# Performance work log

Hardware: AMD Instinct MI355X
Metric: run time of the kernel (lower is better)

Reference implementation:

```python
import jax, jax.numpy as jnp
import numpy as np

D_MODEL = 2048
N_HEADS = 16
D_HEAD = 128
N_GROUPS = 4          # KV heads = N_HEADS // N_GROUPS = 4
D_FF = 2048           # hard-coded default in FeedForward
EPS = 1e-6


def setup_inputs() -> dict:
    key = jax.random.key(0)
    ks = jax.random.split(key, 16)
    B, S = 4, 1024
    Hkv = N_HEADS // N_GROUPS
    s = 0.02
    inp = {
        "x": jax.random.normal(ks[0], (B, S, D_MODEL), jnp.float32),
        "scale1": jnp.ones((D_MODEL,), jnp.float32),
        "Wq": jax.random.normal(ks[1], (D_MODEL, N_HEADS * D_HEAD), jnp.float32) * s,
        "bq": jnp.zeros((N_HEADS * D_HEAD,), jnp.float32),
        "Wk": jax.random.normal(ks[2], (D_MODEL, Hkv * D_HEAD), jnp.float32) * s,
        "bk": jnp.zeros((Hkv * D_HEAD,), jnp.float32),
        "Wv": jax.random.normal(ks[3], (D_MODEL, Hkv * D_HEAD), jnp.float32) * s,
        "bv": jnp.zeros((Hkv * D_HEAD,), jnp.float32),
        "Wo": jax.random.normal(ks[4], (N_HEADS * D_HEAD, D_MODEL), jnp.float32) * s,
        "bo": jnp.zeros((D_MODEL,), jnp.float32),
        "W1": jax.random.normal(ks[5], (D_MODEL, D_FF), jnp.float32) * s,
        "b1": jnp.zeros((D_FF,), jnp.float32),
        "W2": jax.random.normal(ks[6], (D_FF, D_MODEL), jnp.float32) * s,
        "b2": jnp.zeros((D_MODEL,), jnp.float32),
    }
    return inp


def _rmsnorm(x, scale):
    rms = jnp.sqrt(jnp.mean(x * x, axis=-1, keepdims=True) + EPS)
    return scale * (x / rms)


def reference(x, scale1, Wq, bq, Wk, bk, Wv, bv, Wo, bo, W1, b1, W2, b2):
    B, S, _ = x.shape
    Hkv = N_HEADS // N_GROUPS
    xn = _rmsnorm(x, scale1)  # [B,S,D]

    # GQA attention (prefill, step=None -> no cache)
    Q = (xn @ Wq + bq).reshape(B, S, N_HEADS, D_HEAD).transpose(0, 2, 1, 3)  # [B,H,S,d]
    K = (xn @ Wk + bk).reshape(B, S, Hkv, D_HEAD).transpose(0, 2, 1, 3)      # [B,Hkv,S,d]
    V = (xn @ Wv + bv).reshape(B, S, Hkv, D_HEAD).transpose(0, 2, 1, 3)
    Kr = jnp.repeat(K, N_GROUPS, axis=1)  # [B,H,S,d]
    Vr = jnp.repeat(V, N_GROUPS, axis=1)
    scores = jnp.einsum("bhqd,bhkd->bhqk", Q, Kr) / jnp.sqrt(jnp.float32(D_HEAD))
    attn = jax.nn.softmax(scores, axis=-1)
    out = jnp.einsum("bhqk,bhkd->bhqd", attn, Vr)  # [B,H,S,d]
    out = out.transpose(0, 2, 1, 3).reshape(B, S, N_HEADS * D_HEAD)
    x = x + out @ Wo + bo

    # Source bug preserved: FFN consumes rms_norm1 output, rms_norm2 is dead code
    h = xn @ W1 + b1
    h = h * jax.nn.sigmoid(h) * h  # x_ff * silu(x_ff)
    x = x + h @ W2 + b2
    return x
```

## Files before the change

### kernel.cpp

```cpp
#include <hip/hip_runtime.h>
#include <hip/hip_bf16.h>
#include <cstdint>

using bf16 = __hip_bfloat16;
typedef __attribute__((ext_vector_type(8))) __bf16 bf16x8;
typedef __attribute__((ext_vector_type(4))) float f32x4;

#define MFMA16(a, b, c) __builtin_amdgcn_mfma_f32_16x16x32_bf16((a), (b), (c), 0, 0, 0)

#if __has_builtin(__builtin_amdgcn_exp2f)
__device__ __forceinline__ float fexp2(float x) { return __builtin_amdgcn_exp2f(x); }
#else
__device__ __forceinline__ float fexp2(float x) { return exp2f(x); }
#endif

__device__ __forceinline__ void async16(void* lds_ptr, const void* gptr) {
  auto g = reinterpret_cast<__attribute__((address_space(1))) unsigned int*>(
      reinterpret_cast<uintptr_t>(gptr));
  auto l = reinterpret_cast<__attribute__((address_space(3))) unsigned int*>(
      static_cast<unsigned int>(reinterpret_cast<uintptr_t>(lds_ptr)));
  __builtin_amdgcn_global_load_lds(g, l, 16, 0, 0);
}

__device__ __forceinline__ void tr_body(const float* __restrict__ W,
                                        bf16* __restrict__ Wt, int N, int ldt,
                                        int row_off, int k_off, int lb, int nx,
                                        float (*t)[33], int tx, int ty) {
  const int n0 = (lb % nx) * 32, k0 = (lb / nx) * 32;
#pragma unroll
  for (int i = 0; i < 4; ++i)
    t[ty + 8 * i][tx] = W[(size_t)(k0 + ty + 8 * i) * N + n0 + tx];
  __syncthreads();
#pragma unroll
  for (int i = 0; i < 4; ++i)
    Wt[(size_t)(row_off + n0 + ty + 8 * i) * ldt + k_off + k0 + tx] =
        __float2bfloat16(t[tx][ty + 8 * i]);
}

__global__ __launch_bounds__(256) void prep_k(
    const float* __restrict__ x, const float* __restrict__ s1, bf16* __restrict__ xn,
    const float* __restrict__ Wq, const float* __restrict__ Wk,
    const float* __restrict__ Wv, const float* __restrict__ W1,
    const float* __restrict__ Wo, const float* __restrict__ W2,
    bf16* __restrict__ wcatT, bf16* __restrict__ wcat2T,
    const float* __restrict__ bq, const float* __restrict__ bk,
    const float* __restrict__ bv, const float* __restrict__ b1,
    const float* __restrict__ bo, const float* __restrict__ b2,
    float* __restrict__ bcat) {
  __shared__ float t[32][33];
  const int tid = threadIdx.x;
  int bid = blockIdx.x;
  if (bid < 4096) {
    const int row = bid;
    const float4* xr = (const float4*)(x + (size_t)row * 2048);
    float4 a = xr[tid * 2], b = xr[tid * 2 + 1];
    float ss = a.x * a.x + a.y * a.y + a.z * a.z + a.w * a.w +
               b.x * b.x + b.y * b.y + b.z * b.z + b.w * b.w;
#pragma unroll
    for (int d = 1; d < 64; d <<= 1) ss += __shfl_xor(ss, d);
    if ((tid & 63) == 0) t[0][tid >> 6] = ss;
    __syncthreads();
    const float rinv =
        rsqrtf((t[0][0] + t[0][1] + t[0][2] + t[0][3]) * (1.0f / 2048.0f) + 1e-6f);
    const float4* sp = (const float4*)s1;
    float4 s0 = sp[tid * 2], s1v = sp[tid * 2 + 1];
    union { bf16 h[8]; bf16x8 v; } o;
    o.h[0] = __float2bfloat16(a.x * rinv * s0.x);
    o.h[1] = __float2bfloat16(a.y * rinv * s0.y);
    o.h[2] = __float2bfloat16(a.z * rinv * s0.z);
    o.h[3] = __float2bfloat16(a.w * rinv * s0.w);
    o.h[4] = __float2bfloat16(b.x * rinv * s1v.x);
    o.h[5] = __float2bfloat16(b.y * rinv * s1v.y);
    o.h[6] = __float2bfloat16(b.z * rinv * s1v.z);
    o.h[7] = __float2bfloat16(b.w * rinv * s1v.w);
    *(bf16x8*)(xn + (size_t)row * 2048 + tid * 8) = o.v;
    return;
  }
  if (bid < 4124) {
    const int i = (bid - 4096) * 256 + tid;
    float v;
    if (i < 2048) v = bq[i];
    else if (i < 2560) v = bk[i - 2048];
    else if (i < 3072) v = bv[i - 2560];
    else if (i < 5120) v = b1[i - 3072];
    else v = bo[i - 5120] + b2[i - 5120];
    bcat[i] = v;
    return;
  }
  bid -= 4124;
  const int tx = tid & 31, ty = tid >> 5;
  if (bid < 4096)       tr_body(Wq, wcatT, 2048, 2048, 0, 0, bid, 64, t, tx, ty);
  else if (bid < 5120)  tr_body(Wk, wcatT, 512, 2048, 2048, 0, bid - 4096, 16, t, tx, ty);
  else if (bid < 6144)  tr_body(Wv, wcatT, 512, 2048, 2560, 0, bid - 5120, 16, t, tx, ty);
  else if (bid < 10240) tr_body(W1, wcatT, 2048, 2048, 3072, 0, bid - 6144, 64, t, tx, ty);
  else if (bid < 14336) tr_body(Wo, wcat2T, 2048, 4096, 0, 0, bid - 10240, 64, t, tx, ty);
  else                  tr_body(W2, wcat2T, 2048, 4096, 0, 2048, bid - 14336, 64, t, tx, ty);
}

__global__ void transpose_v_k(const bf16* __restrict__ qkv, bf16* __restrict__ vtb) {
  __shared__ bf16 t[32][33];
  const int bh = blockIdx.z, b = bh >> 2, g = bh & 3;
  const int s0 = blockIdx.x * 32, d0 = blockIdx.y * 32;
  const int tx = threadIdx.x, ty = threadIdx.y;
#pragma unroll
  for (int i = 0; i < 4; ++i)
    t[ty + 8 * i][tx] =
        qkv[(size_t)(b * 1024 + s0 + ty + 8 * i) * 3072 + 2560 + g * 128 + d0 + tx];
  __syncthreads();
#pragma unroll
  for (int i = 0; i < 4; ++i)
    vtb[((size_t)bh * 128 + d0 + ty + 8 * i) * 1024 + s0 + tx] = t[tx][ty + 8 * i];
}

#define BARRIER() \
  { asm volatile("" ::: "memory"); __builtin_amdgcn_s_barrier(); asm volatile("" ::: "memory"); }
#define LGKM0() \
  { asm volatile("s_waitcnt lgkmcnt(0)" ::: "memory"); __builtin_amdgcn_sched_barrier(0); }
#define VM_MAIN                                                          \
  { if constexpr (LPS == 4) { asm volatile("s_waitcnt vmcnt(8)" ::: "memory"); } \
    else { asm volatile("s_waitcnt vmcnt(6)" ::: "memory"); }            \
    __builtin_amdgcn_sched_barrier(0); }
#define VM_ONE                                                           \
  { if constexpr (LPS == 4) { asm volatile("s_waitcnt vmcnt(4)" ::: "memory"); } \
    else { asm volatile("s_waitcnt vmcnt(3)" ::: "memory"); }            \
    __builtin_amdgcn_sched_barrier(0); }
#define VM_ZERO \
  { asm volatile("s_waitcnt vmcnt(0)" ::: "memory"); __builtin_amdgcn_sched_barrier(0); }

#define READ_AF(MILO)                                                              \
  { unsigned char* ab_ = lds + (h_ & 3) * SLOTA;                                   \
    _Pragma("unroll") for (int i_ = 0; i_ < MI / 2; ++i_) {                        \
      const int R_ = arow0 + ((MILO) + i_) * 16;                                   \
      af[i_] = *(const bf16x8*)(ab_ + R_ * 64 + ((hi ^ ((R_ >> 1) & 3)) << 4)); } }

#define READ_BF()                                                                  \
  { unsigned char* bb_ = lds + 4 * SLOTA + (h_ & 3) * SLOTB;                       \
    _Pragma("unroll") for (int j_ = 0; j_ < NJ; ++j_) {                            \
      const int S_ = bcol0 + j_ * 16;                                              \
      bf[j_] = *(const bf16x8*)(bb_ + S_ * 64 + ((hi ^ ((S_ >> 1) & 3)) << 4)); } }

#define MFMA_HALF(MILO)                                                            \
  __builtin_amdgcn_s_setprio(1);                                                   \
  _Pragma("unroll") for (int i_ = 0; i_ < MI / 2; ++i_)                            \
    _Pragma("unroll") for (int j_ = 0; j_ < NJ; ++j_)                              \
      acc[(MILO) + i_][j_] = MFMA16(af[i_], bf[j_], acc[(MILO) + i_][j_]);         \
  __builtin_amdgcn_s_setprio(0);

#define GSLOT(H, DOSTG, VMSTMT)                                                    \
  { const int h_ = (H);                                                            \
    READ_AF(0); READ_BF();                                                         \
    if (DOSTG) stgA(h_ + 3);                                                       \
    BARRIER(); LGKM0();                                                            \
    MFMA_HALF(0);                                                                  \
    BARRIER();                                                                     \
    READ_AF(MI / 2);                                                               \
    if (DOSTG) stgB(h_ + 3);                                                       \
    VMSTMT;                                                                        \
    BARRIER(); LGKM0();                                                            \
    MFMA_HALF(MI / 2);                                                             \
    BARRIER(); }

template <int MI, int NJ, int WM, int WN, int EPI>
__global__ __launch_bounds__(512, 2) void gemm8(
    const bf16* __restrict__ A, const bf16* __restrict__ A2,
    const bf16* __restrict__ Bt, const float* __restrict__ bias,
    const float* __restrict__ res, void* __restrict__ out0,
    void* __restrict__ out1, int K) {
  constexpr int BM = WM * MI * 16;
  constexpr int BN = WN * NJ * 16;
  constexpr int SLOTA = BM * 64;
  constexpr int SLOTB = BN * 64;
  constexpr int NSWA = SLOTA / 8192;
  constexpr int NSWB = SLOTB / 8192;
  constexpr int FRACB = SLOTB % 8192;
  constexpr int LPS = NSWA + NSWB;
  extern __shared__ unsigned char lds[];

  const int tid = threadIdx.x, lane = tid & 63, w = tid >> 6;
  const int wr = w / WN, wc = w % WN;
  const int hi = lane >> 4, lo = lane & 15;

  const int lid = blockIdx.y * 16 + blockIdx.x;
  const int xj = lid & 7, jj = lid >> 3;
  const int brow = ((xj & 3) * 4 + (jj & 3)) * BM;
  const int bcol = ((xj >> 2) * 8 + (jj >> 2)) * BN;

  const int NS = K >> 5;

  size_t offA[NSWA];
#pragma unroll
  for (int i = 0; i < NSWA; ++i) {
    const int o = i * 8192 + tid * 16;
    const int r = o >> 6;
    const int c = ((((o >> 4) & 3) ^ ((r >> 1) & 3)) << 3);
    offA[i] = (size_t)(brow + r) * 2048 + c;
  }
  const bf16* srcB[NSWB + (FRACB ? 1 : 0)];
#pragma unroll
  for (int i = 0; i < NSWB + (FRACB ? 1 : 0); ++i) {
    const int o = i * 8192 + tid * 16;
    const int r = o >> 6;
    const int c = ((((o >> 4) & 3) ^ ((r >> 1) & 3)) << 3);
    srcB[i] = Bt + (size_t)(bcol + r) * K + c;
  }

  auto stgA = [&](int h) {
    unsigned char* ab = lds + (h & 3) * SLOTA;
    const int kb = h * 32;
    const bf16* base;
    int ko;
    if constexpr (EPI == 1) { base = (kb < 2048) ? A : A2; ko = kb & 2047; }
    else { base = A; ko = kb; }
#pragma unroll
    for (int i = 0; i < NSWA; ++i)
      async16(ab + i * 8192 + tid * 16, base + offA[i] + ko);
  };
  auto stgB = [&](int h) {
    unsigned char* bb = lds + 4 * SLOTA + (h & 3) * SLOTB;
    const int kb = h * 32;
#pragma unroll
    for (int i = 0; i < NSWB; ++i)
      async16(bb + i * 8192 + tid * 16, srcB[i] + kb);
    if constexpr (FRACB != 0) {
      if (tid < FRACB / 16)
        async16(bb + NSWB * 8192 + tid * 16, srcB[NSWB] + kb);
    }
  };

  const int arow0 = wr * (MI * 16) + lo;
  const int bcol0 = wc * (NJ * 16) + lo;

  stgA(0); stgB(0); stgA(1); stgB(1); stgA(2); stgB(2);
  VM_MAIN;
  BARRIER();

  f32x4 acc[MI][NJ] = {};
  bf16x8 af[MI / 2], bf[NJ];

  for (int h = 0; h < NS - 3; ++h) { GSLOT(h, true, VM_MAIN); }
  GSLOT(NS - 3, false, VM_ONE);
  GSLOT(NS - 2, false, VM_ZERO);
  GSLOT(NS - 1, false, (void)0);

#pragma unroll
  for (int mi = 0; mi < MI; ++mi) {
    const int row = brow + wr * (MI * 16) + mi * 16 + hi * 4;
#pragma unroll
    for (int nj = 0; nj < NJ; ++nj) {
      const int col = bcol + wc * (NJ * 16) + nj * 16 + lo;
      const float bs = bias[col];
#pragma unroll
      for (int r = 0; r < 4; ++r) {
        float v = acc[mi][nj][r] + bs;
        if constexpr (EPI == 0) {
          if (col < 3072) {
            ((bf16*)out0)[(size_t)(row + r) * 3072 + col] = __float2bfloat16(v);
          } else {
            const float sg = 1.0f / (1.0f + __expf(-v));
            ((bf16*)out1)[(size_t)(row + r) * 2048 + (col - 3072)] =
                __float2bfloat16(v * sg * v);
          }
        } else {
          v += res[(size_t)(row + r) * 2048 + col];
          ((float*)out0)[(size_t)(row + r) * 2048 + col] = v;
        }
      }
    }
  }
}

__global__ __launch_bounds__(256, 4) void attn_fwd(
    const bf16* __restrict__ qkv, const bf16* __restrict__ vtb, bf16* __restrict__ out) {
  __shared__ __align__(16) unsigned char alds[40960];
  unsigned char* Ks = alds;
  unsigned char* Vs = alds + 16384;
  unsigned char* Ps = alds + 32768;
  const int tid = threadIdx.x, lane = tid & 63, w = tid >> 6;
  const int hi = lane >> 4, lo = lane & 15;
  const int qt = blockIdx.x, bh = blockIdx.y;
  const int b = bh >> 4, h = bh & 15, g = h >> 2;
  const size_t tok0 = (size_t)b * 1024;
  const int q0 = qt * 64;

  bf16x8 qf[4];
  {
    const bf16* qp = qkv + (tok0 + q0 + w * 16 + lo) * 3072 + h * 128 + hi * 8;
#pragma unroll
    for (int kc = 0; kc < 4; ++kc) qf[kc] = *(const bf16x8*)(qp + kc * 32);
  }

  float m2 = -1e30f, lsum = 0.f;
  f32x4 oacc[8] = {};
  const float c2 = 0.08838834764831845f * 1.44269504088896f;

  const int o = tid * 16;
  const bf16* kbase = qkv + tok0 * 3072 + 2048 + g * 128;
  const bf16* vbase = vtb + (size_t)(b * 4 + g) * 128 * 1024;
  unsigned char* Pw = Ps + w * 2048;

  for (int t = 0; t < 16; ++t) {
    const int kb = t * 64;
#pragma unroll
    for (int rd = 0; rd < 4; ++rd) {
      const int oo = o + rd * 4096;
      const int rK = oo >> 8, cK = ((oo >> 4) & 15) ^ (rK & 15);
      const int rV = oo >> 7, cV = ((oo >> 4) & 7) ^ (rV & 7);
      async16(Ks + oo, kbase + (size_t)(kb + rK) * 3072 + cK * 8);
      async16(Vs + oo, vbase + (size_t)rV * 1024 + kb + cV * 8);
    }
    __syncthreads();

    f32x4 sc[4] = {};
    __builtin_amdgcn_s_setprio(1);
#pragma unroll
    for (int kc = 0; kc < 4; ++kc) {
#pragma unroll
      for (int kg = 0; kg < 4; ++kg) {
        const int row = kg * 16 + lo;
        bf16x8 kf = *(const bf16x8*)(Ks + row * 256 + ((((kc << 2) + hi) ^ (row & 15)) << 4));
        sc[kg] = MFMA16(kf, qf[kc], sc[kg]);
      }
    }
    __builtin_amdgcn_s_setprio(0);

    float mx = sc[0][0];
#pragma unroll
    for (int kg = 0; kg < 4; ++kg)
#pragma unroll
      for (int r = 0; r < 4; ++r) mx = fmaxf(mx, sc[kg][r]);
    mx = fmaxf(mx, __shfl_xor(mx, 16));
    mx = fmaxf(mx, __shfl_xor(mx, 32));
    mx *= c2;
    const float mn = fmaxf(m2, mx);
    const float corr = fexp2(m2 - mn);
    m2 = mn;

    float rs = 0.f;
#pragma unroll
    for (int kg = 0; kg < 4; ++kg) {
      union { bf16 hh[4]; uint2 v; } pk;
#pragma unroll
      for (int r = 0; r < 4; ++r) {
        const float p = fexp2(sc[kg][r] * c2 - mn);
        rs += p;
        pk.hh[r] = __float2bfloat16(p);
      }
      *(uint2*)(Pw + lo * 128 + ((((kg << 1) + (hi >> 1)) ^ (lo & 7)) << 4) +
                ((hi & 1) << 3)) = pk.v;
    }
    rs += __shfl_xor(rs, 16);
    rs += __shfl_xor(rs, 32);
    lsum = lsum * corr + rs;

    float corr_r[4];
#pragma unroll
    for (int r = 0; r < 4; ++r) corr_r[r] = __shfl(corr, hi * 4 + r);
#pragma unroll
    for (int dg = 0; dg < 8; ++dg)
#pragma unroll
      for (int r = 0; r < 4; ++r) oacc[dg][r] *= corr_r[r];

    asm volatile("s_waitcnt lgkmcnt(0)" ::: "memory");

    bf16x8 pf[2];
#pragma unroll
    for (int kc = 0; kc < 2; ++kc)
      pf[kc] = *(const bf16x8*)(Pw + lo * 128 + ((((kc << 2) + hi) ^ (lo & 7)) << 4));
    __builtin_amdgcn_s_setprio(1);
#pragma unroll
    for (int dg = 0; dg < 8; ++dg) {
#pragma unroll
      for (int kc = 0; kc < 2; ++kc) {
        const int vrow = dg * 16 + lo;
        bf16x8 vf = *(const bf16x8*)(Vs + vrow * 128 + ((((kc << 2) + hi) ^ (vrow & 7)) << 4));
        oacc[dg] = MFMA16(pf[kc], vf, oacc[dg]);
      }
    }
    __builtin_amdgcn_s_setprio(0);
    __syncthreads();
  }

  const float linv = 1.0f / lsum;
  float lr[4];
#pragma unroll
  for (int r = 0; r < 4; ++r) lr[r] = __shfl(linv, hi * 4 + r);
  bf16* op = out + (tok0 + q0 + w * 16 + hi * 4) * 2048 + h * 128 + lo;
#pragma unroll
  for (int dg = 0; dg < 8; ++dg)
#pragma unroll
    for (int r = 0; r < 4; ++r)
      op[(size_t)r * 2048 + dg * 16] = __float2bfloat16(oacc[dg][r] * lr[r]);
}

extern "C" void kernel_launch(void* const* d_in, const int* in_sizes, int n_in,
                              void* d_out, int out_size, void* d_ws, size_t ws_size,
                              hipStream_t stream) {
  (void)in_sizes; (void)n_in; (void)out_size; (void)ws_size;
  const float* x  = (const float*)d_in[0];
  const float* s1 = (const float*)d_in[1];
  const float* Wq = (const float*)d_in[2];
  const float* bq = (const float*)d_in[3];
  const float* Wk = (const float*)d_in[4];
  const float* bk = (const float*)d_in[5];
  const float* Wv = (const float*)d_in[6];
  const float* bv = (const float*)d_in[7];
  const float* Wo = (const float*)d_in[8];
  const float* bo = (const float*)d_in[9];
  const float* W1 = (const float*)d_in[10];
  const float* b1 = (const float*)d_in[11];
  const float* W2 = (const float*)d_in[12];
  const float* b2 = (const float*)d_in[13];
  float* outp = (float*)d_out;

  char* ws = (char*)d_ws;
  bf16*  xn     = (bf16*)(ws + 0);
  bf16*  vtb    = (bf16*)(ws + 0);
  bf16*  wcatT  = (bf16*)(ws + 16777216);
  bf16*  attnb  = (bf16*)(ws + 16777216);
  float* bcat   = (float*)(ws + 37748736);
  bf16*  wcat2T = (bf16*)(ws + 37781504);
  bf16*  qkvb   = (bf16*)(ws + 54558720);
  bf16*  gbuf   = (bf16*)(ws + 79724544);

  prep_k<<<dim3(22556), dim3(256), 0, stream>>>(
      x, s1, xn, Wq, Wk, Wv, W1, Wo, W2, wcatT, wcat2T,
      bq, bk, bv, b1, bo, b2, bcat);
  gemm8<8, 5, 2, 4, 0><<<dim3(16, 16), dim3(512), 147456, stream>>>(
      xn, xn, wcatT, bcat, (const float*)nullptr, (void*)qkvb, (void*)gbuf, 2048);
  transpose_v_k<<<dim3(32, 4, 16), dim3(32, 8), 0, stream>>>(qkvb, vtb);
  attn_fwd<<<dim3(16, 64), dim3(256), 0, stream>>>(qkvb, vtb, attnb);
  gemm8<4, 4, 4, 2, 1><<<dim3(16, 16), dim3(512), 98304, stream>>>(
      attnb, gbuf, wcat2T, bcat + 5120, x, (void*)outp, (void*)nullptr, 4096);
}
```

Measured before the change: 240.8 us.

## Split output GEMM into per-source K halves with 256x256 tiles plus reduce

The final projection GEMM, previously one K=4096 pass over the concatenated attention and FFN activations with 256x128 tiles, becomes a new kernel. It uses 256x256 tiles and splits K into the attention half and the FFN half as separate blocks, each writing a bf16 partial product. A separate elementwise kernel then sums both partials with the residual and bias into the fp32 output. Larger tiles are meant to cut redundant operand loads from global memory and LDS per FLOP. The cost is an extra round trip of two bf16 partial buffers and an extra launch, and rounding the partials to bf16 before summing costs some accuracy.

Measured after the change: 243.3 us. About the same (+1.1%).

```diff
diff --git a/kernel.cpp b/kernel.cpp
--- a/kernel.cpp
+++ b/kernel.cpp
@@ -21,6 +21,11 @@
       static_cast<unsigned int>(reinterpret_cast<uintptr_t>(lds_ptr)));
   __builtin_amdgcn_global_load_lds(g, l, 16, 0, 0);
 }
+
+#define BARRIER() \
+  { asm volatile("" ::: "memory"); __builtin_amdgcn_s_barrier(); asm volatile("" ::: "memory"); }
+#define LGKM0() \
+  { asm volatile("s_waitcnt lgkmcnt(0)" ::: "memory"); __builtin_amdgcn_sched_barrier(0); }
 
 __device__ __forceinline__ void tr_body(const float* __restrict__ W,
                                         bf16* __restrict__ Wt, int N, int ldt,
@@ -112,10 +117,6 @@
     vtb[((size_t)bh * 128 + d0 + ty + 8 * i) * 1024 + s0 + tx] = t[tx][ty + 8 * i];
 }
 
-#define BARRIER() \
-  { asm volatile("" ::: "memory"); __builtin_amdgcn_s_barrier(); asm volatile("" ::: "memory"); }
-#define LGKM0() \
-  { asm volatile("s_waitcnt lgkmcnt(0)" ::: "memory"); __builtin_amdgcn_sched_barrier(0); }
 #define VM_MAIN                                                          \
   { if constexpr (LPS == 4) { asm volatile("s_waitcnt vmcnt(8)" ::: "memory"); } \
     else { asm volatile("s_waitcnt vmcnt(6)" ::: "memory"); }            \
@@ -160,11 +161,10 @@
     MFMA_HALF(MI / 2);                                                             \
     BARRIER(); }
 
-template <int MI, int NJ, int WM, int WN, int EPI>
+template <int MI, int NJ, int WM, int WN>
 __global__ __launch_bounds__(512, 2) void gemm8(
-    const bf16* __restrict__ A, const bf16* __restrict__ A2,
-    const bf16* __restrict__ Bt, const float* __restrict__ bias,
-    const float* __restrict__ res, void* __restrict__ out0,
+    const bf16* __restrict__ A, const bf16* __restrict__ Bt,
+    const float* __restrict__ bias, void* __restrict__ out0,
     void* __restrict__ out1, int K) {
   constexpr int BM = WM * MI * 16;
   constexpr int BN = WN * NJ * 16;
@@ -207,13 +207,9 @@
   auto stgA = [&](int h) {
     unsigned char* ab = lds + (h & 3) * SLOTA;
     const int kb = h * 32;
-    const bf16* base;
-    int ko;
-    if constexpr (EPI == 1) { base = (kb < 2048) ? A : A2; ko = kb & 2047; }
-    else { base = A; ko = kb; }
 #pragma unroll
     for (int i = 0; i < NSWA; ++i)
-      async16(ab + i * 8192 + tid * 16, base + offA[i] + ko);
+      async16(ab + i * 8192 + tid * 16, A + offA[i] + kb);
   };
   auto stgB = [&](int h) {
     unsigned char* bb = lds + 4 * SLOTA + (h & 3) * SLOTB;
@@ -252,20 +248,152 @@
 #pragma unroll
       for (int r = 0; r < 4; ++r) {
         float v = acc[mi][nj][r] + bs;
-        if constexpr (EPI == 0) {
-          if (col < 3072) {
-            ((bf16*)out0)[(size_t)(row + r) * 3072 + col] = __float2bfloat16(v);
-          } else {
-            const float sg = 1.0f / (1.0f + __expf(-v));
-            ((bf16*)out1)[(size_t)(row + r) * 2048 + (col - 3072)] =
-                __float2bfloat16(v * sg * v);
-          }
+        if (col < 3072) {
+          ((bf16*)out0)[(size_t)(row + r) * 3072 + col] = __float2bfloat16(v);
         } else {
-          v += res[(size_t)(row + r) * 2048 + col];
-          ((float*)out0)[(size_t)(row + r) * 2048 + col] = v;
+          const float sg = 1.0f / (1.0f + __expf(-v));
+          ((bf16*)out1)[(size_t)(row + r) * 2048 + (col - 3072)] =
+              __float2bfloat16(v * sg * v);
         }
       }
     }
+  }
+}
+
+#define PH_RDA(Q)                                                               \
+  _Pragma("unroll") for (int i = 0; i < 4; ++i)                                 \
+    _Pragma("unroll") for (int k = 0; k < 2; ++k) {                             \
+      const int R = wr * 128 + ((Q) + i) * 16 + lo;                             \
+      af[i][k] = *(const bf16x8*)(lds + ((2 * j + k) & 3) * 16384 + R * 64 +    \
+                                  ((hi ^ ((R >> 1) & 3)) << 4));                \
+    }
+#define PH_RDB(H)                                                               \
+  _Pragma("unroll") for (int n = 0; n < 2; ++n)                                 \
+    _Pragma("unroll") for (int k = 0; k < 2; ++k) {                             \
+      const int R = wc * 64 + ((H) + n) * 16 + lo;                              \
+      bf[(H) + n][k] = *(const bf16x8*)(lds + 65536 +                           \
+                                  ((2 * j + k) & 3) * 16384 + R * 64 +          \
+                                  ((hi ^ ((R >> 1) & 3)) << 4));                \
+    }
+#define PH_MM(Q, H)                                                             \
+  __builtin_amdgcn_s_setprio(1);                                                \
+  _Pragma("unroll") for (int i = 0; i < 4; ++i)                                 \
+    _Pragma("unroll") for (int n = 0; n < 2; ++n)                               \
+      _Pragma("unroll") for (int k = 0; k < 2; ++k)                             \
+        acc[(Q) + i][(H) + n] =                                                 \
+            MFMA16(af[i][k], bf[(H) + n][k], acc[(Q) + i][(H) + n]);            \
+  __builtin_amdgcn_s_setprio(0);
+
+__global__ __launch_bounds__(512, 2) void gemm_ph(
+    const bf16* __restrict__ Az0, const bf16* __restrict__ Az1,
+    const bf16* __restrict__ Bt, bf16* __restrict__ P0b,
+    bf16* __restrict__ P1b) {
+  extern __shared__ unsigned char lds[];
+  const int tid = threadIdx.x, lane = tid & 63, w = tid >> 6;
+  const int wr = w >> 2, wc = w & 3;
+  const int hi = lane >> 4, lo = lane & 15;
+  const int lid = (blockIdx.z * 8 + blockIdx.y) * 16 + blockIdx.x;
+  const int xj = lid & 7, jj = lid >> 3;
+  const int z = xj >> 2;
+  const int brow = ((xj & 3) * 4 + (jj & 3)) * 256;
+  const int bcol = (jj >> 2) * 256;
+  const bf16* Ab = z ? Az1 : Az0;
+  bf16* Pb = z ? P1b : P0b;
+  const size_t koff = (size_t)z * 2048;
+
+  size_t offA[2], offB[2];
+#pragma unroll
+  for (int s = 0; s < 2; ++s) {
+    const int o = s * 8192 + tid * 16;
+    const int r = o >> 6;
+    const int c = ((o >> 4) & 3) ^ ((r >> 1) & 3);
+    offA[s] = (size_t)(brow + r) * 2048 + c * 8;
+    offB[s] = (size_t)(bcol + r) * 4096 + koff + c * 8;
+  }
+  auto stgA = [&](int t, int kk) {
+    unsigned char* sb = lds + (((t << 1) + kk) & 3) * 16384;
+    const int kb = t * 64 + kk * 32;
+#pragma unroll
+    for (int s = 0; s < 2; ++s)
+      async16(sb + s * 8192 + tid * 16, Ab + offA[s] + kb);
+  };
+  auto stgB = [&](int t, int kk) {
+    unsigned char* sb = lds + 65536 + (((t << 1) + kk) & 3) * 16384;
+    const int kb = t * 64 + kk * 32;
+#pragma unroll
+    for (int s = 0; s < 2; ++s)
+      async16(sb + s * 8192 + tid * 16, Bt + offB[s] + kb);
+  };
+
+  f32x4 acc[8][4] = {};
+  bf16x8 af[4][2], bf[4][2];
+
+  stgA(0, 0); stgA(0, 1); stgB(0, 0); stgB(0, 1); stgB(1, 0); stgB(1, 1);
+  asm volatile("s_waitcnt vmcnt(4)" ::: "memory");
+  BARRIER();
+
+  for (int j = 0; j < 30; ++j) {
+    PH_RDA(0); PH_RDB(0); stgA(j + 1, 0);
+    BARRIER(); LGKM0(); PH_MM(0, 0); BARRIER();
+    PH_RDB(2); stgA(j + 1, 1);
+    BARRIER(); LGKM0(); PH_MM(0, 2); BARRIER();
+    PH_RDA(4); stgB(j + 2, 0);
+    BARRIER(); LGKM0(); PH_MM(4, 2); BARRIER();
+    stgB(j + 2, 1);
+    asm volatile("s_waitcnt vmcnt(4)" ::: "memory");
+    BARRIER(); PH_MM(4, 0); BARRIER();
+  }
+  {
+    const int j = 30;
+    PH_RDA(0); PH_RDB(0); stgA(31, 0);
+    BARRIER(); LGKM0(); PH_MM(0, 0); BARRIER();
+    PH_RDB(2); stgA(31, 1);
+    BARRIER(); LGKM0(); PH_MM(0, 2); BARRIER();
+    PH_RDA(4);
+    BARRIER(); LGKM0(); PH_MM(4, 2); BARRIER();
+    asm volatile("s_waitcnt vmcnt(0)" ::: "memory");
+    BARRIER(); PH_MM(4, 0); BARRIER();
+  }
+  {
+    const int j = 31;
+    PH_RDA(0); PH_RDB(0);
+    BARRIER(); LGKM0(); PH_MM(0, 0); BARRIER();
+    PH_RDB(2);
+    BARRIER(); LGKM0(); PH_MM(0, 2); BARRIER();
+    PH_RDA(4);
+    BARRIER(); LGKM0(); PH_MM(4, 2); BARRIER();
+    PH_MM(4, 0);
+  }
+
+#pragma unroll
+  for (int mi = 0; mi < 8; ++mi) {
+    const int row0 = brow + wr * 128 + mi * 16 + hi * 4;
+#pragma unroll
+    for (int nj = 0; nj < 4; ++nj) {
+      const int col = bcol + wc * 64 + nj * 16 + lo;
+#pragma unroll
+      for (int r = 0; r < 4; ++r)
+        Pb[(size_t)(row0 + r) * 2048 + col] = __float2bfloat16(acc[mi][nj][r]);
+    }
+  }
+}
+
+__global__ __launch_bounds__(256) void reduce_k(
+    const float* __restrict__ x, const bf16* __restrict__ P0,
+    const bf16* __restrict__ P1, const float* __restrict__ bias,
+    float* __restrict__ out) {
+  const int n4 = 4096 * 2048 / 4;
+  for (int i = blockIdx.x * 256 + threadIdx.x; i < n4; i += gridDim.x * 256) {
+    float4 xv = ((const float4*)x)[i];
+    ushort4 a = ((const ushort4*)P0)[i];
+    ushort4 b = ((const ushort4*)P1)[i];
+    float4 bv = ((const float4*)bias)[i & 511];
+    float4 o;
+    o.x = xv.x + __uint_as_float((unsigned)a.x << 16) + __uint_as_float((unsigned)b.x << 16) + bv.x;
+    o.y = xv.y + __uint_as_float((unsigned)a.y << 16) + __uint_as_float((unsigned)b.y << 16) + bv.y;
+    o.z = xv.z + __uint_as_float((unsigned)a.z << 16) + __uint_as_float((unsigned)b.z << 16) + bv.z;
+    o.w = xv.w + __uint_as_float((unsigned)a.w << 16) + __uint_as_float((unsigned)b.w << 16) + bv.w;
+    ((float4*)out)[i] = o;
   }
 }
 
@@ -415,20 +543,22 @@
   char* ws = (char*)d_ws;
   bf16*  xn     = (bf16*)(ws + 0);
   bf16*  vtb    = (bf16*)(ws + 0);
+  bf16*  P0     = (bf16*)(ws + 0);
   bf16*  wcatT  = (bf16*)(ws + 16777216);
   bf16*  attnb  = (bf16*)(ws + 16777216);
   float* bcat   = (float*)(ws + 37748736);
   bf16*  wcat2T = (bf16*)(ws + 37781504);
   bf16*  qkvb   = (bf16*)(ws + 54558720);
+  bf16*  P1     = (bf16*)(ws + 54558720);
   bf16*  gbuf   = (bf16*)(ws + 79724544);
 
   prep_k<<<dim3(22556), dim3(256), 0, stream>>>(
       x, s1, xn, Wq, Wk, Wv, W1, Wo, W2, wcatT, wcat2T,
       bq, bk, bv, b1, bo, b2, bcat);
-  gemm8<8, 5, 2, 4, 0><<<dim3(16, 16), dim3(512), 147456, stream>>>(
-      xn, xn, wcatT, bcat, (const float*)nullptr, (void*)qkvb, (void*)gbuf, 2048);
+  gemm8<8, 5, 2, 4><<<dim3(16, 16), dim3(512), 147456, stream>>>(
+      xn, wcatT, bcat, (void*)qkvb, (void*)gbuf, 2048);
   transpose_v_k<<<dim3(32, 4, 16), dim3(32, 8), 0, stream>>>(qkvb, vtb);
   attn_fwd<<<dim3(16, 64), dim3(256), 0, stream>>>(qkvb, vtb, attnb);
-  gemm8<4, 4, 4, 2, 1><<<dim3(16, 16), dim3(512), 98304, stream>>>(
-      attnb, gbuf, wcat2T, bcat + 5120, x, (void*)outp, (void*)nullptr, 4096);
-}
+  gemm_ph<<<dim3(16, 8, 2), dim3(512), 131072, stream>>>(attnb, gbuf, wcat2T, P0, P1);
+  reduce_k<<<dim3(2048), dim3(256), 0, stream>>>(x, P0, P1, bcat + 5120, outp);
+}
```

## Switch GEMM kernels from 16x16x32 to 32x32x16 bf16 MFMA tiles

Applied to the files above, without the earlier changes.

Rewrites the pipelined GEMM so each wave computes 32x32 output tiles with the 32x32x16 bf16 MFMA instead of 16x16x32. The wave layout is fixed at 4x2 with BM=256, and the LDS fragment reads and the epilogue indexing are reworked for the larger MFMA layout. The goal is fewer LDS fragment reads per FLOP and higher MFMA efficiency. The cost is larger accumulator register pressure and a new, less coalesced epilogue store pattern.

After: 258.8 us. +7.5%, slower.

```diff
diff --git a/kernel.cpp b/kernel.cpp
--- a/kernel.cpp
+++ b/kernel.cpp
@@ -5,8 +5,10 @@
 using bf16 = __hip_bfloat16;
 typedef __attribute__((ext_vector_type(8))) __bf16 bf16x8;
 typedef __attribute__((ext_vector_type(4))) float f32x4;
+typedef __attribute__((ext_vector_type(16))) float f32x16;
 
 #define MFMA16(a, b, c) __builtin_amdgcn_mfma_f32_16x16x32_bf16((a), (b), (c), 0, 0, 0)
+#define MFMA32(a, b, c) __builtin_amdgcn_mfma_f32_32x32x16_bf16((a), (b), (c), 0, 0, 0)
 
 #if __has_builtin(__builtin_amdgcn_exp2f)
 __device__ __forceinline__ float fexp2(float x) { return __builtin_amdgcn_exp2f(x); }
@@ -21,6 +23,11 @@
       static_cast<unsigned int>(reinterpret_cast<uintptr_t>(lds_ptr)));
   __builtin_amdgcn_global_load_lds(g, l, 16, 0, 0);
 }
+
+#define BARRIER() \
+  { asm volatile("" ::: "memory"); __builtin_amdgcn_s_barrier(); asm volatile("" ::: "memory"); }
+#define LGKM0() \
+  { asm volatile("s_waitcnt lgkmcnt(0)" ::: "memory"); __builtin_amdgcn_sched_barrier(0); }
 
 __device__ __forceinline__ void tr_body(const float* __restrict__ W,
                                         bf16* __restrict__ Wt, int N, int ldt,
@@ -112,10 +119,6 @@
     vtb[((size_t)bh * 128 + d0 + ty + 8 * i) * 1024 + s0 + tx] = t[tx][ty + 8 * i];
 }
 
-#define BARRIER() \
-  { asm volatile("" ::: "memory"); __builtin_amdgcn_s_barrier(); asm volatile("" ::: "memory"); }
-#define LGKM0() \
-  { asm volatile("s_waitcnt lgkmcnt(0)" ::: "memory"); __builtin_amdgcn_sched_barrier(0); }
 #define VM_MAIN                                                          \
   { if constexpr (LPS == 4) { asm volatile("s_waitcnt vmcnt(8)" ::: "memory"); } \
     else { asm volatile("s_waitcnt vmcnt(6)" ::: "memory"); }            \
@@ -127,47 +130,46 @@
 #define VM_ZERO \
   { asm volatile("s_waitcnt vmcnt(0)" ::: "memory"); __builtin_amdgcn_sched_barrier(0); }
 
-#define READ_AF(MILO)                                                              \
+#define R32_A(TT)                                                                  \
   { unsigned char* ab_ = lds + (h_ & 3) * SLOTA;                                   \
-    _Pragma("unroll") for (int i_ = 0; i_ < MI / 2; ++i_) {                        \
-      const int R_ = arow0 + ((MILO) + i_) * 16;                                   \
-      af[i_] = *(const bf16x8*)(ab_ + R_ * 64 + ((hi ^ ((R_ >> 1) & 3)) << 4)); } }
-
-#define READ_BF()                                                                  \
+    _Pragma("unroll") for (int kk = 0; kk < 2; ++kk)                               \
+      af[kk] = *(const bf16x8*)(ab_ + (arow + (TT) * 32) * 64 + swzA[kk]); }
+
+#define R32_B()                                                                    \
   { unsigned char* bb_ = lds + 4 * SLOTA + (h_ & 3) * SLOTB;                       \
-    _Pragma("unroll") for (int j_ = 0; j_ < NJ; ++j_) {                            \
-      const int S_ = bcol0 + j_ * 16;                                              \
-      bf[j_] = *(const bf16x8*)(bb_ + S_ * 64 + ((hi ^ ((S_ >> 1) & 3)) << 4)); } }
-
-#define MFMA_HALF(MILO)                                                            \
+    _Pragma("unroll") for (int nt = 0; nt < NT; ++nt)                              \
+      _Pragma("unroll") for (int kk = 0; kk < 2; ++kk)                             \
+        bf[nt][kk] = *(const bf16x8*)(bb_ + (scol + nt * 32) * 64 + swzB[kk]); }
+
+#define MM32(TT)                                                                   \
   __builtin_amdgcn_s_setprio(1);                                                   \
-  _Pragma("unroll") for (int i_ = 0; i_ < MI / 2; ++i_)                            \
-    _Pragma("unroll") for (int j_ = 0; j_ < NJ; ++j_)                              \
-      acc[(MILO) + i_][j_] = MFMA16(af[i_], bf[j_], acc[(MILO) + i_][j_]);         \
+  _Pragma("unroll") for (int nt = 0; nt < NT; ++nt)                                \
+    _Pragma("unroll") for (int kk = 0; kk < 2; ++kk)                               \
+      acc[TT][nt] = MFMA32(af[kk], bf[nt][kk], acc[TT][nt]);                       \
   __builtin_amdgcn_s_setprio(0);
 
 #define GSLOT(H, DOSTG, VMSTMT)                                                    \
   { const int h_ = (H);                                                            \
-    READ_AF(0); READ_BF();                                                         \
+    R32_A(0); R32_B();                                                             \
     if (DOSTG) stgA(h_ + 3);                                                       \
     BARRIER(); LGKM0();                                                            \
-    MFMA_HALF(0);                                                                  \
+    MM32(0);                                                                       \
     BARRIER();                                                                     \
-    READ_AF(MI / 2);                                                               \
+    R32_A(1);                                                                      \
     if (DOSTG) stgB(h_ + 3);                                                       \
     VMSTMT;                                                                        \
     BARRIER(); LGKM0();                                                            \
-    MFMA_HALF(MI / 2);                                                             \
+    MM32(1);                                                                       \
     BARRIER(); }
 
-template <int MI, int NJ, int WM, int WN, int EPI>
-__global__ __launch_bounds__(512, 2) void gemm8(
+template <int NT, int EPI>
+__global__ __launch_bounds__(512, 2) void gemm32(
     const bf16* __restrict__ A, const bf16* __restrict__ A2,
     const bf16* __restrict__ Bt, const float* __restrict__ bias,
     const float* __restrict__ res, void* __restrict__ out0,
     void* __restrict__ out1, int K) {
-  constexpr int BM = WM * MI * 16;
-  constexpr int BN = WN * NJ * 16;
+  constexpr int BM = 256;
+  constexpr int BN = 2 * NT * 32;
   constexpr int SLOTA = BM * 64;
   constexpr int SLOTB = BN * 64;
   constexpr int NSWA = SLOTA / 8192;
@@ -177,8 +179,8 @@
   extern __shared__ unsigned char lds[];
 
   const int tid = threadIdx.x, lane = tid & 63, w = tid >> 6;
-  const int wr = w / WN, wc = w % WN;
-  const int hi = lane >> 4, lo = lane & 15;
+  const int wr = w >> 1, wc = w & 1;
+  const int l31 = lane & 31, ln5 = lane >> 5;
 
   const int lid = blockIdx.y * 16 + blockIdx.x;
   const int xj = lid & 7, jj = lid >> 3;
@@ -227,15 +229,21 @@
     }
   };
 
-  const int arow0 = wr * (MI * 16) + lo;
-  const int bcol0 = wc * (NJ * 16) + lo;
+  const int arow = wr * 64 + l31;
+  const int scol = wc * (NT * 32) + l31;
+  int swzA[2], swzB[2];
+#pragma unroll
+  for (int kk = 0; kk < 2; ++kk) {
+    swzA[kk] = (((kk << 1) + ln5) ^ ((arow >> 1) & 3)) << 4;
+    swzB[kk] = (((kk << 1) + ln5) ^ ((scol >> 1) & 3)) << 4;
+  }
 
   stgA(0); stgB(0); stgA(1); stgB(1); stgA(2); stgB(2);
   VM_MAIN;
   BARRIER();
 
-  f32x4 acc[MI][NJ] = {};
-  bf16x8 af[MI / 2], bf[NJ];
+  f32x16 acc[2][NT] = {};
+  bf16x8 af[2], bf[NT][2];
 
   for (int h = 0; h < NS - 3; ++h) { GSLOT(h, true, VM_MAIN); }
   GSLOT(NS - 3, false, VM_ONE);
@@ -243,26 +251,30 @@
   GSLOT(NS - 1, false, (void)0);
 
 #pragma unroll
-  for (int mi = 0; mi < MI; ++mi) {
-    const int row = brow + wr * (MI * 16) + mi * 16 + hi * 4;
-#pragma unroll
-    for (int nj = 0; nj < NJ; ++nj) {
-      const int col = bcol + wc * (NJ * 16) + nj * 16 + lo;
+  for (int mt = 0; mt < 2; ++mt) {
+#pragma unroll
+    for (int nt = 0; nt < NT; ++nt) {
+      const int col = bcol + wc * (NT * 32) + nt * 32 + l31;
       const float bs = bias[col];
 #pragma unroll
-      for (int r = 0; r < 4; ++r) {
-        float v = acc[mi][nj][r] + bs;
-        if constexpr (EPI == 0) {
-          if (col < 3072) {
-            ((bf16*)out0)[(size_t)(row + r) * 3072 + col] = __float2bfloat16(v);
+      for (int g = 0; g < 4; ++g) {
+        const int row0 = brow + wr * 64 + mt * 32 + g * 8 + ln5 * 4;
+#pragma unroll
+        for (int q = 0; q < 4; ++q) {
+          float v = acc[mt][nt][g * 4 + q] + bs;
+          const int row = row0 + q;
+          if constexpr (EPI == 0) {
+            if (col < 3072) {
+              ((bf16*)out0)[(size_t)row * 3072 + col] = __float2bfloat16(v);
+            } else {
+              const float sg = 1.0f / (1.0f + __expf(-v));
+              ((bf16*)out1)[(size_t)row * 2048 + (col - 3072)] =
+                  __float2bfloat16(v * sg * v);
+            }
           } else {
-            const float sg = 1.0f / (1.0f + __expf(-v));
-            ((bf16*)out1)[(size_t)(row + r) * 2048 + (col - 3072)] =
-                __float2bfloat16(v * sg * v);
+            v += res[(size_t)row * 2048 + col];
+            ((float*)out0)[(size_t)row * 2048 + col] = v;
           }
-        } else {
-          v += res[(size_t)(row + r) * 2048 + col];
-          ((float*)out0)[(size_t)(row + r) * 2048 + col] = v;
         }
       }
     }
@@ -425,10 +437,10 @@
   prep_k<<<dim3(22556), dim3(256), 0, stream>>>(
       x, s1, xn, Wq, Wk, Wv, W1, Wo, W2, wcatT, wcat2T,
       bq, bk, bv, b1, bo, b2, bcat);
-  gemm8<8, 5, 2, 4, 0><<<dim3(16, 16), dim3(512), 147456, stream>>>(
+  gemm32<5, 0><<<dim3(16, 16), dim3(512), 147456, stream>>>(
       xn, xn, wcatT, bcat, (const float*)nullptr, (void*)qkvb, (void*)gbuf, 2048);
   transpose_v_k<<<dim3(32, 4, 16), dim3(32, 8), 0, stream>>>(qkvb, vtb);
   attn_fwd<<<dim3(16, 64), dim3(256), 0, stream>>>(qkvb, vtb, attnb);
-  gemm8<4, 4, 4, 2, 1><<<dim3(16, 16), dim3(512), 98304, stream>>>(
+  gemm32<2, 1><<<dim3(16, 16), dim3(512), 98304, stream>>>(
       attnb, gbuf, wcat2T, bcat + 5120, x, (void*)outp, (void*)nullptr, 4096);
 }
```
